# Kernel tuning notes

Hardware: AMD Instinct MI355X
Metric: run time of the kernel (lower is better)

## Reference

```python
import jax, jax.numpy as jnp
import numpy as np

TAU1, TAU2, TSCALE = 30.0, 5.0, 6.0   # tau1 > tau2, in frame units (hz=None)
B, T_OUT = 1000, 20000                # neurons x output frames


def _biexp_kernel():
    # exact replica of SpikeToCalcium.set_double_exp
    r = TAU1 / TAU2
    d = TAU1 - TAU2
    scale = np.power(r, -TAU2 / d) - np.power(r, -TAU1 / d)
    t = np.arange(1.0, TAU1 * TSCALE + 2.0, dtype=np.float32)  # 181 taps
    e1 = np.exp(-t / TAU1)
    e2 = np.exp(-t / TAU2)
    return ((e1 - e2) / scale).astype(np.float32)


def setup_inputs() -> dict:
    key = jax.random.key(0)
    kernel = jnp.asarray(_biexp_kernel())           # (181,)
    Kt = kernel.shape[0]
    u = jax.random.normal(key, (B, T_OUT + Kt - 1), dtype=jnp.float32)  # (1000, 20180)
    return {"u": u, "kernel": kernel}


def reference(u, kernel):
    # Original: K.conv1d(u[..., None], kernel[::-1, None, None], 1, 'valid')
    # keras conv1d is cross-correlation; reversing the kernel makes it a true
    # causal FIR convolution. lax.conv_general_dilated is also cross-correlation,
    # so we pass the reversed kernel identically.
    rhs = kernel[::-1][None, None, :]               # (O=1, I=1, K)
    lhs = u[:, None, :]                             # (B, C=1, T_in)
    out = jax.lax.conv_general_dilated(
        lhs, rhs, window_strides=(1,), padding='VALID',
        dimension_numbers=('NCH', 'OIH', 'NCH'))
    return out[:, 0, :]                             # (B, T_in - K + 1)
```

## Files before the change

kernel.cpp:

```cpp
#include <hip/hip_runtime.h>
#include <hip/hip_bf16.h>

namespace {
constexpr int kB   = 1000;
constexpr int kT   = 20000;
constexpr int kKt  = 181;
constexpr int kInW = kT + kKt - 1;
constexpr int TW     = 128;
constexpr int NTILE  = TW / 16;
constexpr int NFRAG  = NTILE + 12;
constexpr int NB     = (kB + 15) / 16;
constexpr int NS     = (kT + TW - 1) / TW;
constexpr int NJOBS  = NB * NS;
constexpr int WPB    = 4;
constexpr int NBLK   = (NJOBS + WPB - 1) / WPB;

typedef short bf16x8 __attribute__((ext_vector_type(8)));
typedef float f32x4  __attribute__((ext_vector_type(4)));

__device__ __forceinline__ unsigned pack_bf16x2(float lo, float hi) {
  __hip_bfloat162 h = __float22bfloat162_rn(float2{lo, hi});
  unsigned w;
  __builtin_memcpy(&w, &h, 4);
  return w;
}

template <bool B> struct TailTag { static constexpr bool value = B; };
}

__global__ __launch_bounds__(256, 3)
void biexp_stream(const float* __restrict__ u, const float* __restrict__ kern,
                  float* __restrict__ out) {
  __shared__ float lds_k[kKt];
  const int tid = threadIdx.x;
  if (tid < kKt) lds_k[tid] = kern[tid];
  __syncthreads();

  const int lane = tid & 63;
  const int wave = tid >> 6;
  const int quad = lane >> 4;
  const int nn   = lane & 15;

  union { bf16x8 v; unsigned w[4]; } bfr[7];
  #pragma unroll
  for (int c = 0; c < 7; ++c) {
    #pragma unroll
    for (int jj = 0; jj < 4; ++jj) {
      int i0 = 32 * c + quad * 8 + 2 * jj - nn;
      float f0 = (i0 >= 0     && i0 < kKt)     ? lds_k[kKt - 1 - i0] : 0.0f;
      float f1 = (i0 + 1 >= 0 && i0 + 1 < kKt) ? lds_k[kKt - 2 - i0] : 0.0f;
      bfr[c].w[jj] = pack_bf16x2(f0, f1);
    }
  }

  const int job = blockIdx.x * WPB + wave;
  if (job >= NJOBS) return;
  const int jb = job / NS;
  const int js = job - jb * NS;
  const int b0 = jb * 16;
  const int t0 = js * TW;

  const int row = min(b0 + nn, kB - 1);
  const float* __restrict__ urow = u + (size_t)row * kInW;

  auto body = [&](auto tail_tag) {
    constexpr bool TAIL = decltype(tail_tag)::value;
    auto load_frag = [&](int m) -> bf16x8 {
      int col = t0 + 16 * m + quad * 8;
      union { bf16x8 v; unsigned w[4]; } r;
      if (!TAIL || col + 8 <= kInW) {
        f32x4 a = *(const f32x4*)(urow + col);
        f32x4 b = *(const f32x4*)(urow + col + 4);
        r.w[0] = pack_bf16x2(a[0], a[1]);
        r.w[1] = pack_bf16x2(a[2], a[3]);
        r.w[2] = pack_bf16x2(b[0], b[1]);
        r.w[3] = pack_bf16x2(b[2], b[3]);
      } else {
        float e[8];
        #pragma unroll
        for (int j = 0; j < 8; ++j) e[j] = urow[min(col + j, kInW - 1)];
        r.w[0] = pack_bf16x2(e[0], e[1]);
        r.w[1] = pack_bf16x2(e[2], e[3]);
        r.w[2] = pack_bf16x2(e[4], e[5]);
        r.w[3] = pack_bf16x2(e[6], e[7]);
      }
      return r.v;
    };

    bf16x8 F[NFRAG];
    #pragma unroll
    for (int m = 0; m < 14; ++m) F[m] = load_frag(m);

    #pragma unroll
    for (int jt = 0; jt < NTILE; ++jt) {
      if (jt + 14 < NFRAG) F[jt + 14] = load_frag(jt + 14);
      f32x4 acc0 = {0.f, 0.f, 0.f, 0.f};
      f32x4 acc1 = {0.f, 0.f, 0.f, 0.f};
      #pragma unroll
      for (int c = 0; c < 7; c += 2)
        acc0 = __builtin_amdgcn_mfma_f32_16x16x32_bf16(F[jt + 2 * c], bfr[c].v, acc0, 0, 0, 0);
      #pragma unroll
      for (int c = 1; c < 7; c += 2)
        acc1 = __builtin_amdgcn_mfma_f32_16x16x32_bf16(F[jt + 2 * c], bfr[c].v, acc1, 0, 0, 0);
      const int gt = t0 + 16 * jt + nn;
      if (gt < kT) {
        #pragma unroll
        for (int r = 0; r < 4; ++r) {
          const int gb = b0 + quad * 4 + r;
          if (gb < kB) out[(size_t)gb * kT + gt] = acc0[r] + acc1[r];
        }
      }
    }
  };

  if (js == NS - 1) body(TailTag<true>{});
  else              body(TailTag<false>{});
}

extern "C" void kernel_launch(void* const* d_in, const int* in_sizes, int n_in,
                              void* d_out, int out_size, void* d_ws, size_t ws_size,
                              hipStream_t stream) {
  const float* u  = (const float*)d_in[0];
  const float* kn = (const float*)d_in[1];
  float* out = (float*)d_out;
  hipLaunchKernelGGL(biexp_stream, dim3(NBLK, 1, 1), dim3(256, 1, 1), 0, stream,
                     u, kn, out);
}
```

Before: 162.9 us.

## Stage input strips through triple-buffered LDS with register-prefetch pipeline

Replaces per-wave direct global fragment loads with a block-cooperative pipeline. Each block stages 16-row by 256-column bf16 strips into a triple-buffered LDS ring, and the next-next strip is prefetched into registers while MFMAs run on the current one. The four waves share the staged input, which removes the per-wave halo reloads, and a manual bf16 rounding routine is added. In exchange the kernel adds LDS traffic, a block barrier every strip, and higher occupancy bounds that may force register spills.

```diff
diff --git a/kernel.cpp b/kernel.cpp
--- a/kernel.cpp
+++ b/kernel.cpp
@@ -6,14 +6,14 @@
 constexpr int kT   = 20000;
 constexpr int kKt  = 181;
 constexpr int kInW = kT + kKt - 1;
-constexpr int TW     = 128;
-constexpr int NTILE  = TW / 16;
-constexpr int NFRAG  = NTILE + 12;
-constexpr int NB     = (kB + 15) / 16;
-constexpr int NS     = (kT + TW - 1) / TW;
-constexpr int NJOBS  = NB * NS;
-constexpr int WPB    = 4;
-constexpr int NBLK   = (NJOBS + WPB - 1) / WPB;
+constexpr int CH     = 256;
+constexpr int STRIDE = CH + 8;
+constexpr int SLOT   = 16 * STRIDE;
+constexpr int SPB    = 4;
+constexpr int NSTRIP = (kT + CH - 1) / CH;
+constexpr int NSG    = (NSTRIP + SPB - 1) / SPB;
+constexpr int NBG    = (kB + 15) / 16;
+constexpr int NBLK   = NBG * NSG;
 
 typedef short bf16x8 __attribute__((ext_vector_type(8)));
 typedef float f32x4  __attribute__((ext_vector_type(4)));
@@ -24,26 +24,70 @@
   __builtin_memcpy(&w, &h, 4);
   return w;
 }
-
-template <bool B> struct TailTag { static constexpr bool value = B; };
+__device__ __forceinline__ short f32_bf16(float f) {
+  union { float f; unsigned u; } x; x.f = f;
+  unsigned r = x.u + (0x7fffu + ((x.u >> 16) & 1u));
+  return (short)(r >> 16);
+}
 }
 
-__global__ __launch_bounds__(256, 3)
-void biexp_stream(const float* __restrict__ u, const float* __restrict__ kern,
-                  float* __restrict__ out) {
+__global__ __launch_bounds__(256, 5)
+void biexp_pipe(const float* __restrict__ u, const float* __restrict__ kern,
+                float* __restrict__ out) {
+  __shared__ short lds_a[3 * SLOT];
   __shared__ float lds_k[kKt];
+
   const int tid = threadIdx.x;
   if (tid < kKt) lds_k[tid] = kern[tid];
-  __syncthreads();
+
+  const int bx = blockIdx.x;
+  const int jb = bx % NBG;
+  const int sg = bx / NBG;
+  const int b0 = jb * 16;
+  const int s0 = sg * SPB;
 
   const int lane = tid & 63;
   const int wave = tid >> 6;
   const int quad = lane >> 4;
   const int nn   = lane & 15;
 
+  const int srow = tid >> 4;
+  const int scol = (tid & 15) * 4;
+  const float* __restrict__ srcrow = u + (size_t)min(b0 + srow, kB - 1) * kInW;
+
+  auto issue = [&](int c, f32x4 v[4]) {
+    const int base = CH * c + scol;
+    if (CH * (c + 1) <= kInW) {
+      #pragma unroll
+      for (int i = 0; i < 4; ++i) v[i] = *(const f32x4*)(srcrow + base + 64 * i);
+    } else {
+      #pragma unroll
+      for (int i = 0; i < 4; ++i)
+        #pragma unroll
+        for (int j = 0; j < 4; ++j) v[i][j] = srcrow[min(base + 64 * i + j, kInW - 1)];
+    }
+  };
+  auto commit = [&](int c, const f32x4 v[4]) {
+    short* dst = &lds_a[(c % 3) * SLOT + srow * STRIDE + scol];
+    #pragma unroll
+    for (int i = 0; i < 4; ++i) {
+      short4 s;
+      s.x = f32_bf16(v[i][0]); s.y = f32_bf16(v[i][1]);
+      s.z = f32_bf16(v[i][2]); s.w = f32_bf16(v[i][3]);
+      *(short4*)(dst + 64 * i) = s;
+    }
+  };
+
+  f32x4 vA[4], vB[4];
+  issue(s0, vA);
+  issue(s0 + 1, vB);
+  commit(s0, vA);
+  commit(s0 + 1, vB);
+  __syncthreads();
+
   union { bf16x8 v; unsigned w[4]; } bfr[7];
   #pragma unroll
-  for (int c = 0; c < 7; ++c) {
+  for (int c = 0; c < 7; ++c)
     #pragma unroll
     for (int jj = 0; jj < 4; ++jj) {
       int i0 = 32 * c + quad * 8 + 2 * jj - nn;
@@ -51,70 +95,43 @@
       float f1 = (i0 + 1 >= 0 && i0 + 1 < kKt) ? lds_k[kKt - 2 - i0] : 0.0f;
       bfr[c].w[jj] = pack_bf16x2(f0, f1);
     }
-  }
 
-  const int job = blockIdx.x * WPB + wave;
-  if (job >= NJOBS) return;
-  const int jb = job / NS;
-  const int js = job - jb * NS;
-  const int b0 = jb * 16;
-  const int t0 = js * TW;
+  const int colw = 64 * wave + 8 * quad;
+  for (int k = 0; k < SPB; ++k) {
+    const int s = s0 + k;
+    if (s >= NSTRIP) break;
+    const bool pf = (k + 1 < SPB) && (s + 1 < NSTRIP);
+    if (pf) issue(s + 2, vA);
 
-  const int row = min(b0 + nn, kB - 1);
-  const float* __restrict__ urow = u + (size_t)row * kInW;
-
-  auto body = [&](auto tail_tag) {
-    constexpr bool TAIL = decltype(tail_tag)::value;
-    auto load_frag = [&](int m) -> bf16x8 {
-      int col = t0 + 16 * m + quad * 8;
-      union { bf16x8 v; unsigned w[4]; } r;
-      if (!TAIL || col + 8 <= kInW) {
-        f32x4 a = *(const f32x4*)(urow + col);
-        f32x4 b = *(const f32x4*)(urow + col + 4);
-        r.w[0] = pack_bf16x2(a[0], a[1]);
-        r.w[1] = pack_bf16x2(a[2], a[3]);
-        r.w[2] = pack_bf16x2(b[0], b[1]);
-        r.w[3] = pack_bf16x2(b[2], b[3]);
-      } else {
-        float e[8];
-        #pragma unroll
-        for (int j = 0; j < 8; ++j) e[j] = urow[min(col + j, kInW - 1)];
-        r.w[0] = pack_bf16x2(e[0], e[1]);
-        r.w[1] = pack_bf16x2(e[2], e[3]);
-        r.w[2] = pack_bf16x2(e[4], e[5]);
-        r.w[3] = pack_bf16x2(e[6], e[7]);
-      }
-      return r.v;
-    };
-
-    bf16x8 F[NFRAG];
-    #pragma unroll
-    for (int m = 0; m < 14; ++m) F[m] = load_frag(m);
+    const int T0 = s * CH;
+    const int slotA = (s % 3) * SLOT;
+    const int slotB = ((s + 1) % 3) * SLOT;
+    const short* lrow = &lds_a[nn * STRIDE];
 
     #pragma unroll
-    for (int jt = 0; jt < NTILE; ++jt) {
-      if (jt + 14 < NFRAG) F[jt + 14] = load_frag(jt + 14);
+    for (int jt = 0; jt < 4; ++jt) {
       f32x4 acc0 = {0.f, 0.f, 0.f, 0.f};
       f32x4 acc1 = {0.f, 0.f, 0.f, 0.f};
       #pragma unroll
-      for (int c = 0; c < 7; c += 2)
-        acc0 = __builtin_amdgcn_mfma_f32_16x16x32_bf16(F[jt + 2 * c], bfr[c].v, acc0, 0, 0, 0);
+      for (int c = 0; c < 7; ++c) {
+        const int off = colw + 16 * jt + 32 * c;
+        const int within = off & 255;
+        const short* p = lrow + ((off >> 8) ? slotB : slotA) + within;
+        bf16x8 a = *(const bf16x8*)p;
+        if (c & 1) acc1 = __builtin_amdgcn_mfma_f32_16x16x32_bf16(a, bfr[c].v, acc1, 0, 0, 0);
+        else       acc0 = __builtin_amdgcn_mfma_f32_16x16x32_bf16(a, bfr[c].v, acc0, 0, 0, 0);
+      }
+      const int gt = T0 + 64 * wave + 16 * jt + nn;
       #pragma unroll
-      for (int c = 1; c < 7; c += 2)
-        acc1 = __builtin_amdgcn_mfma_f32_16x16x32_bf16(F[jt + 2 * c], bfr[c].v, acc1, 0, 0, 0);
-      const int gt = t0 + 16 * jt + nn;
-      if (gt < kT) {
-        #pragma unroll
-        for (int r = 0; r < 4; ++r) {
-          const int gb = b0 + quad * 4 + r;
-          if (gb < kB) out[(size_t)gb * kT + gt] = acc0[r] + acc1[r];
-        }
+      for (int r = 0; r < 4; ++r) {
+        const int gb = b0 + quad * 4 + r;
+        if (gb < kB && gt < kT) out[(size_t)gb * kT + gt] = acc0[r] + acc1[r];
       }
     }
-  };
 
-  if (js == NS - 1) body(TailTag<true>{});
-  else              body(TailTag<false>{});
+    if (pf) commit(s + 2, vA);
+    __syncthreads();
+  }
 }
 
 extern "C" void kernel_launch(void* const* d_in, const int* in_sizes, int n_in,
@@ -123,6 +140,6 @@
   const float* u  = (const float*)d_in[0];
   const float* kn = (const float*)d_in[1];
   float* out = (float*)d_out;
-  hipLaunchKernelGGL(biexp_stream, dim3(NBLK, 1, 1), dim3(256, 1, 1), 0, stream,
+  hipLaunchKernelGGL(biexp_pipe, dim3(NBLK, 1, 1), dim3(256, 1, 1), 0, stream,
                      u, kn, out);
 }
```

Result: slower. 245.4 us (+50.6%).
